# Kernel tuning notes

Hardware: AMD Instinct MI355X
Metric: run time of the kernel (lower is better)

Reference implementation:

```python
import jax, jax.numpy as jnp
import numpy as np

D, H, DK, L, FF = 512, 8, 64, 6, 2048
MAXREL = 512
R = 2 * MAXREL + 1
B, S = 4, 512


def _ln(x, g, b):
    m = jnp.mean(x, -1, keepdims=True)
    v = jnp.mean((x - m) ** 2, -1, keepdims=True)
    return (x - m) * jax.lax.rsqrt(v + 1e-5) * g + b


def _gelu(x):
    return jax.nn.gelu(x, approximate=False)


def setup_inputs() -> dict:
    key = jax.random.key(0)
    ks = iter(jax.random.split(key, 64))
    def rnd(shape, scale=0.02):
        return jax.random.normal(next(ks), shape, jnp.float32) * scale
    inp = {"x": jax.random.normal(next(ks), (B, S, D), jnp.float32)}
    # SeasonalDecomposition params (3 seasonal nets stacked on leading axis)
    inp.update(
        sd_t1_w=rnd((D, D)), sd_t1_b=jnp.zeros((D,), jnp.float32),
        sd_t2_w=rnd((D, D)), sd_t2_b=jnp.zeros((D,), jnp.float32),
        sd_s1_w=rnd((3, D, D // 2)), sd_s1_b=jnp.zeros((3, D // 2), jnp.float32),
        sd_s2_w=rnd((3, D // 2, D)), sd_s2_b=jnp.zeros((3, D), jnp.float32),
        sd_r1_w=rnd((D, D // 2)), sd_r1_b=jnp.zeros((D // 2,), jnp.float32),
        sd_r2_w=rnd((D // 2, D)), sd_r2_b=jnp.zeros((D,), jnp.float32),
        sd_comb=jnp.ones((5,), jnp.float32),
        # 6 TemporalFusionTransformer layers, params stacked on leading axis L
        wq=rnd((L, D, D)), wk=rnd((L, D, D)), wv=rnd((L, D, D)),
        wo_w=rnd((L, D, D)), wo_b=jnp.zeros((L, D), jnp.float32),
        rel_k=rnd((L, R, DK), 1.0), rel_v=rnd((L, R, DK), 1.0),
        ln_attn_g=jnp.ones((L, D), jnp.float32), ln_attn_b=jnp.zeros((L, D), jnp.float32),
        ff1_w=rnd((L, D, FF)), ff1_b=jnp.zeros((L, FF), jnp.float32),
        ff2_w=rnd((L, FF, D)), ff2_b=jnp.zeros((L, D), jnp.float32),
        n1_g=jnp.ones((L, D), jnp.float32), n1_b=jnp.zeros((L, D), jnp.float32),
        n2_g=jnp.ones((L, D), jnp.float32), n2_b=jnp.zeros((L, D), jnp.float32),
    )
    return inp


def _forward(x, sd_t1_w, sd_t1_b, sd_t2_w, sd_t2_b, sd_s1_w, sd_s1_b, sd_s2_w, sd_s2_b,
             sd_r1_w, sd_r1_b, sd_r2_w, sd_r2_b, sd_comb,
             wq, wk, wv, wo_w, wo_b, rel_k, rel_v, ln_attn_g, ln_attn_b,
             ff1_w, ff1_b, ff2_w, ff2_b, n1_g, n1_b, n2_g, n2_b):
    b, s, d = x.shape
    # relative position index matrix, rp[i, j] = clip(j - i) + MAXREL
    r = jnp.arange(s)
    rp = jnp.clip(r[None, :] - r[:, None], -MAXREL, MAXREL) + MAXREL  # [S, S]

    # ---- SeasonalDecomposition (eval mode: dropout = identity) ----
    trend = _gelu(x @ sd_t1_w + sd_t1_b) @ sd_t2_w + sd_t2_b
    h = _gelu(jnp.einsum('bsd,kdm->kbsm', x, sd_s1_w) + sd_s1_b[:, None, None, :])
    seas = jnp.einsum('kbsm,kmd->kbsd', h, sd_s2_w) + sd_s2_b[:, None, None, :]  # [3,B,S,D]
    resid = _gelu(x @ sd_r1_w + sd_r1_b) @ sd_r2_w + sd_r2_b
    w = jax.nn.softmax(sd_comb)
    x = w[0] * trend + w[4] * resid + jnp.einsum('k,kbsd->bsd', w[1:4], seas)

    scale = np.float32(1.0 / np.sqrt(DK))

    def layer(xc, p):
        q = (xc @ p['wq']).reshape(b, s, H, DK).transpose(0, 2, 1, 3)  # [B,H,S,DK]
        k = (xc @ p['wk']).reshape(b, s, H, DK).transpose(0, 2, 1, 3)
        v = (xc @ p['wv']).reshape(b, s, H, DK).transpose(0, 2, 1, 3)
        scores = jnp.einsum('bhid,bhjd->bhij', q, k) * scale
        rk = p['rel_k'][rp]  # [S,S,DK] gathered rel-pos key bias
        scores = scores + jnp.einsum('bhid,ijd->bhij', q, rk)
        a = jax.nn.softmax(scores, axis=-1)
        ctx = jnp.einsum('bhij,bhjd->bhid', a, v)
        rv = p['rel_v'][rp]  # [S,S,DK]
        ctx = ctx + jnp.einsum('bhij,ijd->bhid', a, rv)
        ctx = ctx.transpose(0, 2, 1, 3).reshape(b, s, d)
        out = ctx @ p['wo_w'] + p['wo_b']
        attn = _ln(out + xc, p['ln_attn_g'], p['ln_attn_b'])
        y = _ln(xc + attn, p['n1_g'], p['n1_b'])
        ff = _gelu(y @ p['ff1_w'] + p['ff1_b']) @ p['ff2_w'] + p['ff2_b']
        y = _ln(y + ff, p['n2_g'], p['n2_b'])
        return y, None

    layers = dict(wq=wq, wk=wk, wv=wv, wo_w=wo_w, wo_b=wo_b, rel_k=rel_k, rel_v=rel_v,
                  ln_attn_g=ln_attn_g, ln_attn_b=ln_attn_b,
                  ff1_w=ff1_w, ff1_b=ff1_b, ff2_w=ff2_w, ff2_b=ff2_b,
                  n1_g=n1_g, n1_b=n1_b, n2_g=n2_g, n2_b=n2_b)
    x, _ = jax.lax.scan(layer, x, layers)
    return x


def reference(x, sd_t1_w, sd_t1_b, sd_t2_w, sd_t2_b, sd_s1_w, sd_s1_b, sd_s2_w, sd_s2_b,
              sd_r1_w, sd_r1_b, sd_r2_w, sd_r2_b, sd_comb,
              wq, wk, wv, wo_w, wo_b, rel_k, rel_v, ln_attn_g, ln_attn_b,
              ff1_w, ff1_b, ff2_w, ff2_b, n1_g, n1_b, n2_g, n2_b):
    return _forward(x, sd_t1_w, sd_t1_b, sd_t2_w, sd_t2_b, sd_s1_w, sd_s1_b, sd_s2_w, sd_s2_b,
                    sd_r1_w, sd_r1_b, sd_r2_w, sd_r2_b, sd_comb,
                    wq, wk, wv, wo_w, wo_b, rel_k, rel_v, ln_attn_g, ln_attn_b,
                    ff1_w, ff1_b, ff2_w, ff2_b, n1_g, n1_b, n2_g, n2_b)
```

## Files before the change

### kernel.cpp

```cpp
#include <hip/hip_runtime.h>
#include <hip/hip_bf16.h>

typedef __attribute__((ext_vector_type(4))) float f32x4;
typedef __attribute__((ext_vector_type(8))) short bf16x8;
typedef __attribute__((ext_vector_type(4))) short bf16x4;

#define NL 6

static __device__ __forceinline__ unsigned short f2bf(float f) {
    __hip_bfloat16 h = __float2bfloat16(f);
    return *reinterpret_cast<unsigned short*>(&h);
}
static __device__ __forceinline__ float bf2f(unsigned short u) {
    union { unsigned int u32; float f; } c; c.u32 = ((unsigned int)u) << 16; return c.f;
}
static __device__ __forceinline__ float gelu_exact(float v) {
    return 0.5f * v * (1.0f + erff(v * 0.70710678118654752f));
}
static __device__ __forceinline__ void gload_lds16(const void* g, void* l) {
    __builtin_amdgcn_global_load_lds((const __attribute__((address_space(1))) void*)g,
                                     (__attribute__((address_space(3))) void*)l, 16, 0, 0);
}
static __device__ __forceinline__ f32x4 MF(bf16x8 a, bf16x8 b, f32x4 c) {
    return __builtin_amdgcn_mfma_f32_16x16x32_bf16(a, b, c, 0, 0, 0);
}

template<int BM, int BN, bool OBF, bool BIAS, bool GACT, bool SPART, bool DUAL>
__global__ __launch_bounds__(256)
void gemm3(const unsigned short* __restrict__ A, const unsigned short* __restrict__ B,
           void* __restrict__ C, unsigned short* __restrict__ C2,
           const float* __restrict__ bias,
           int M, int N, int nkt, int skN, int lda, int ldb, int ldc, float alpha,
           int modA, long sA1, long sA2, int modB, long sB1, long sB2,
           int modC, long sC1, long sC2, int biasStride, long pStride)
{
    constexpr int MI = BM / 32, NI = BN / 32;
    constexpr int ACH = BM / 8, NCH = (BM + BN) / 8;
    __shared__ __attribute__((aligned(16))) unsigned short Ls[(BM + BN) * 64];

    const int bz = blockIdx.z;
    const int sk = SPART ? (bz % skN) : 0;
    const int z  = SPART ? (bz / skN) : bz;
    const unsigned short* Ab = A + (long)(z % modA) * sA1 + (long)(z / modA) * sA2;
    const unsigned short* Bb = B + (long)(z % modB) * sB1 + (long)(z / modB) * sB2;
    const long offC = (long)(z % modC) * sC1 + (long)(z / modC) * sC2;

    const int bm0 = blockIdx.x * BM, bn0 = blockIdx.y * BN;
    const int t = threadIdx.x, lane = t & 63, w = t >> 6;
    const int wm = (w >> 1) * (BM / 2), wn = (w & 1) * (BN / 2);
    const int crow8 = lane >> 3, cs8 = lane & 7;
    const int fr = lane & 15, kq = lane >> 4;
    const int kBase = sk * nkt * 64;

    f32x4 acc[MI][NI];
    #pragma unroll
    for (int a = 0; a < MI; a++)
        #pragma unroll
        for (int b = 0; b < NI; b++) acc[a][b] = (f32x4){0.f, 0.f, 0.f, 0.f};

    for (int kt = 0; kt < nkt; ++kt) {
        const int k0 = kBase + (kt << 6);
        #pragma unroll
        for (int c0 = 0; c0 < NCH; c0 += 4) {
            int c = c0 + w;
            if (c < NCH) {
                const unsigned short* gp;
                if (c < ACH) {
                    int rit = c * 8 + crow8;
                    int ks = cs8 ^ (rit & 7);
                    gp = Ab + (long)(bm0 + rit) * lda + k0 + ks * 8;
                } else {
                    int rit = (c - ACH) * 8 + crow8;
                    int ks = cs8 ^ (rit & 7);
                    gp = Bb + (long)(bn0 + rit) * ldb + k0 + ks * 8;
                }
                gload_lds16(gp, &Ls[c * 512]);
            }
        }
        __syncthreads();
        bf16x8 af[2][MI], bfr[2][NI];
        #pragma unroll
        for (int mi = 0; mi < MI; mi++) {
            int R = wm + mi * 16 + fr;
            af[0][mi] = *(const bf16x8*)&Ls[R * 64 + ((kq ^ (R & 7)) << 3)];
            af[1][mi] = *(const bf16x8*)&Ls[R * 64 + (((4 + kq) ^ (R & 7)) << 3)];
        }
        #pragma unroll
        for (int ni = 0; ni < NI; ni++) {
            int Rb = wn + ni * 16 + fr;
            bfr[0][ni] = *(const bf16x8*)&Ls[BM * 64 + Rb * 64 + ((kq ^ (Rb & 7)) << 3)];
            bfr[1][ni] = *(const bf16x8*)&Ls[BM * 64 + Rb * 64 + (((4 + kq) ^ (Rb & 7)) << 3)];
        }
        #pragma unroll
        for (int kh = 0; kh < 2; kh++)
            #pragma unroll
            for (int mi = 0; mi < MI; mi++)
                #pragma unroll
                for (int ni = 0; ni < NI; ni++)
                    acc[mi][ni] = MF(af[kh][mi], bfr[kh][ni], acc[mi][ni]);
        __syncthreads();
    }

    const int q4 = (lane >> 4) << 2;
    if (SPART) {
        float* P = (float*)C + sk * pStride + offC;
        #pragma unroll
        for (int mi = 0; mi < MI; mi++)
            #pragma unroll
            for (int ni = 0; ni < NI; ni++)
                #pragma unroll
                for (int j = 0; j < 4; j++) {
                    int gr = bm0 + wm + mi * 16 + q4 + j;
                    int gc = bn0 + wn + ni * 16 + fr;
                    if (gc < N) P[(long)gr * ldc + gc] = acc[mi][ni][j] * alpha;
                }
    } else {
        float* Cf = (float*)C + offC;
        unsigned short* Ch = (unsigned short*)C + offC;
        unsigned short* C2h = DUAL ? (C2 + offC) : nullptr;
        const float* bp = BIAS ? (bias + (long)z * biasStride) : nullptr;
        #pragma unroll
        for (int mi = 0; mi < MI; mi++)
            #pragma unroll
            for (int ni = 0; ni < NI; ni++)
                #pragma unroll
                for (int j = 0; j < 4; j++) {
                    int gr = bm0 + wm + mi * 16 + q4 + j;
                    int gc = bn0 + wn + ni * 16 + fr;
                    if (gc < N) {
                        float v = acc[mi][ni][j] * alpha;
                        if (BIAS) v += bp[gc];
                        if (GACT) v = gelu_exact(v);
                        if (OBF) Ch[(long)gr * ldc + gc] = f2bf(v);
                        else     Cf[(long)gr * ldc + gc] = v;
                        if (DUAL) C2h[(long)gr * ldc + gc] = f2bf(v);
                    }
                }
    }
}

__global__ __launch_bounds__(256)
void fused_attn2(const unsigned short* __restrict__ qkv,
                 const unsigned short* __restrict__ vt,
                 const unsigned short* __restrict__ rk,
                 const unsigned short* __restrict__ rvt,
                 unsigned short* __restrict__ ctx)
{
    __shared__ __attribute__((aligned(16))) unsigned short L[65536];
    const int bh = blockIdx.y, b = bh >> 3, h = bh & 7;
    const int i0 = blockIdx.x * 64;
    const int t = threadIdx.x, lane = t & 63, wv = t >> 6;
    const int crow = lane >> 2, cs = lane & 3;
    const int fr = lane & 15, kq = lane >> 4;
    const int q4 = kq << 2;
    const int iiw = wv * 16;
    const int PB = 53248, GA = 57344;

    const unsigned short* Qg = qkv + ((long)(b * 512 + i0)) * 1536 + h * 64;
    const unsigned short* Kg = qkv + ((long)(b * 512)) * 1536 + 512 + h * 64;
    const unsigned short* Vg = vt + ((long)bh * 64) * 512;

    auto stage = [&](int jt, int sbuf) {
        const int j0 = jt * 64, rbase = j0 - i0 + 448;
        const int SB = 4096 + sbuf * 24576;
        #pragma unroll
        for (int k = 0; k < 12; k++) {
            int c = wv + k * 4;
            const unsigned short* gp; int dst;
            if (c < 8) {
                int kt = c >> 2, row = (c & 3) * 16 + crow, ks = cs ^ (row & 3);
                gp = Kg + (long)(j0 + row) * 1536 + kt * 32 + ks * 8;
                dst = SB + c * 512;
            } else if (c < 16) {
                int cc = c - 8;
                int kt = cc >> 2, row = (cc & 3) * 16 + crow, ks = cs ^ (row & 3);
                gp = Vg + (long)row * 512 + j0 + kt * 32 + ks * 8;
                dst = SB + 4096 + cc * 512;
            } else if (c < 32) {
                int cc = c - 16;
                int kt = cc >> 2, row = (cc & 3) * 16 + crow, ks = cs ^ (row & 3);
                gp = rvt + (long)row * 1056 + rbase + kt * 32 + ks * 8;
                dst = SB + 8192 + cc * 512;
            } else {
                int cc = c - 32;
                int kt = cc >> 3, row = (cc & 7) * 16 + crow, ks = cs ^ (row & 3);
                gp = rk + (long)(rbase + row) * 64 + kt * 32 + ks * 8;
                dst = SB + 16384 + cc * 512;
            }
            gload_lds16(gp, &L[dst]);
        }
    };

    #pragma unroll
    for (int k = 0; k < 2; k++) {
        int c = wv + k * 4;
        int kt = c >> 2, row = (c & 3) * 16 + crow, ks = cs ^ (row & 3);
        gload_lds16(Qg + (long)row * 1536 + kt * 32 + ks * 8, &L[c * 512]);
    }
    stage(0, 0);
    __syncthreads();
    bf16x8 qf[2];
    {
        int r = iiw + fr;
        qf[0] = *(const bf16x8*)&L[r * 32 + ((kq ^ (r & 3)) << 3)];
        qf[1] = *(const bf16x8*)&L[2048 + r * 32 + ((kq ^ (r & 3)) << 3)];
    }

    f32x4 ctxa[4];
    #pragma unroll
    for (int ni = 0; ni < 4; ni++) ctxa[ni] = (f32x4){0.f, 0.f, 0.f, 0.f};
    float m_[4] = {-1e30f, -1e30f, -1e30f, -1e30f};
    float l_[4] = {0.f, 0.f, 0.f, 0.f};

    for (int jt = 0; jt < 8; ++jt) {
        const int sb = jt & 1;
        const int SB = 4096 + sb * 24576;
        if (jt < 7) stage(jt + 1, sb ^ 1);
        f32x4 gacc[8];
        #pragma unroll
        for (int wb = 0; wb < 8; wb++) {
            int Rb = wb * 16 + fr;
            bf16x8 rk0 = *(const bf16x8*)&L[SB + 16384 + Rb * 32 + ((kq ^ (Rb & 3)) << 3)];
            bf16x8 rk1 = *(const bf16x8*)&L[SB + 20480 + Rb * 32 + ((kq ^ (Rb & 3)) << 3)];
            f32x4 g = (f32x4){0.f, 0.f, 0.f, 0.f};
            g = MF(qf[0], rk0, g);
            gacc[wb] = MF(qf[1], rk1, g);
        }
        #pragma unroll
        for (int wb = 0; wb < 8; wb++)
            #pragma unroll
            for (int j = 0; j < 4; j++) {
                int il = iiw + q4 + j, ww = wb * 16 + fr;
                L[GA + il * 128 + (((ww >> 3) ^ (il & 7)) << 3) + (ww & 7)] = f2bf(gacc[wb][j]);
            }
        f32x4 s[4];
        #pragma unroll
        for (int ni = 0; ni < 4; ni++) {
            int rB = ni * 16 + fr;
            bf16x8 b0 = *(const bf16x8*)&L[SB + rB * 32 + ((kq ^ (rB & 3)) << 3)];
            bf16x8 b1 = *(const bf16x8*)&L[SB + 2048 + rB * 32 + ((kq ^ (rB & 3)) << 3)];
            f32x4 a0 = (f32x4){0.f, 0.f, 0.f, 0.f};
            a0 = MF(qf[0], b0, a0);
            s[ni] = MF(qf[1], b1, a0);
        }
        #pragma unroll
        for (int ni = 0; ni < 4; ni++)
            #pragma unroll
            for (int j = 0; j < 4; j++) {
                int il = iiw + q4 + j;
                int ww = ni * 16 + fr - il + 64;
                s[ni][j] = s[ni][j] * 0.125f
                         + bf2f(L[GA + il * 128 + (((ww >> 3) ^ (il & 7)) << 3) + (ww & 7)]);
            }
        float mx[4];
        #pragma unroll
        for (int j = 0; j < 4; j++) {
            mx[j] = fmaxf(fmaxf(s[0][j], s[1][j]), fmaxf(s[2][j], s[3][j]));
            #pragma unroll
            for (int msk = 1; msk < 16; msk <<= 1) mx[j] = fmaxf(mx[j], __shfl_xor(mx[j], msk));
        }
        float scl[4];
        #pragma unroll
        for (int j = 0; j < 4; j++) {
            float mn = fmaxf(m_[j], mx[j]);
            scl[j] = __expf(m_[j] - mn);
            m_[j] = mn;
        }
        float rs[4] = {0.f, 0.f, 0.f, 0.f};
        #pragma unroll
        for (int ni = 0; ni < 4; ni++)
            #pragma unroll
            for (int j = 0; j < 4; j++) {
                float p = __expf(s[ni][j] - m_[j]);
                s[ni][j] = p;
                rs[j] += p;
            }
        #pragma unroll
        for (int j = 0; j < 4; j++) {
            #pragma unroll
            for (int msk = 1; msk < 16; msk <<= 1) rs[j] += __shfl_xor(rs[j], msk);
            l_[j] = l_[j] * scl[j] + rs[j];
        }
        #pragma unroll
        for (int ni = 0; ni < 4; ni++)
            #pragma unroll
            for (int j = 0; j < 4; j++) ctxa[ni][j] *= scl[j];
        #pragma unroll
        for (int ni = 0; ni < 4; ni++)
            #pragma unroll
            for (int j = 0; j < 4; j++) {
                int il = iiw + q4 + j;
                int jj = ni * 16 + fr;
                unsigned short pb = f2bf(s[ni][j]);
                L[PB + il * 64 + (((jj >> 3) ^ (il & 7)) << 3) + (jj & 7)] = pb;
                int wI = jj - il + 64;
                L[GA + il * 128 + (((wI >> 3) ^ (il & 7)) << 3) + (wI & 7)] = pb;
                int wz = (wI + 64) & 127;
                L[GA + il * 128 + (((wz >> 3) ^ (il & 7)) << 3) + (wz & 7)] = 0;
            }
        const int r = iiw + fr;
        bf16x8 pa0 = *(const bf16x8*)&L[PB + r * 64 + ((kq ^ (r & 7)) << 3)];
        bf16x8 pa1 = *(const bf16x8*)&L[PB + r * 64 + (((4 + kq) ^ (r & 7)) << 3)];
        #pragma unroll
        for (int ni = 0; ni < 4; ni++) {
            int rB = ni * 16 + fr;
            bf16x8 vb0 = *(const bf16x8*)&L[SB + 4096 + rB * 32 + ((kq ^ (rB & 3)) << 3)];
            bf16x8 vb1 = *(const bf16x8*)&L[SB + 6144 + rB * 32 + ((kq ^ (rB & 3)) << 3)];
            ctxa[ni] = MF(pa0, vb0, ctxa[ni]);
            ctxa[ni] = MF(pa1, vb1, ctxa[ni]);
        }
        #pragma unroll
        for (int kt2 = 0; kt2 < 4; kt2++) {
            bf16x8 aa = *(const bf16x8*)&L[GA + r * 128 + (((kt2 * 4 + kq) ^ (r & 7)) << 3)];
            #pragma unroll
            for (int ni = 0; ni < 4; ni++) {
                int rB = ni * 16 + fr;
                bf16x8 rb = *(const bf16x8*)&L[SB + 8192 + kt2 * 2048 + rB * 32 + ((kq ^ (rB & 3)) << 3)];
                ctxa[ni] = MF(aa, rb, ctxa[ni]);
            }
        }
        __syncthreads();
    }
    #pragma unroll
    for (int j = 0; j < 4; j++) {
        float inv = 1.f / l_[j];
        int il = iiw + q4 + j;
        unsigned short* op = ctx + ((long)(b * 512 + i0 + il)) * 512 + h * 64;
        #pragma unroll
        for (int ni = 0; ni < 4; ni++)
            op[ni * 16 + fr] = f2bf(ctxa[ni][j] * inv);
    }
}

__global__ __launch_bounds__(256)
void trcast_k(const float* __restrict__ in, unsigned short* __restrict__ out,
              int R, int C, int ldo, long inStride, long outStride,
              const float* __restrict__ scp, int sczs)
{
    __shared__ unsigned short tile[32][33];
    const int z = blockIdx.z;
    const float* ip = in + (long)z * inStride;
    unsigned short* op = out + (long)z * outStride;
    const float sc = scp ? scp[z * sczs] : 1.0f;
    const int c0 = blockIdx.x * 32, r0 = blockIdx.y * 32;
    const int tx = threadIdx.x & 31, ty = threadIdx.x >> 5;
    #pragma unroll
    for (int q = 0; q < 4; q++) {
        int r = r0 + ty + q * 8;
        float v = (r < R) ? ip[(long)r * C + c0 + tx] * sc : 0.f;
        tile[ty + q * 8][tx] = f2bf(v);
    }
    __syncthreads();
    #pragma unroll
    for (int q = 0; q < 4; q++) {
        int c = c0 + ty + q * 8;
        op[(long)c * ldo + r0 + tx] = tile[tx][ty + q * 8];
    }
}

__global__ __launch_bounds__(256)
void qkvwo_tr(const float* __restrict__ wq, const float* __restrict__ wk,
              const float* __restrict__ wv, const float* __restrict__ wo,
              unsigned short* __restrict__ qkvT, unsigned short* __restrict__ woT)
{
    __shared__ unsigned short tile[32][33];
    const int z = blockIdx.z;
    const int which = z >> 1 >> 1 >> 0;
    const int wsel = z / 6, l = z % 6;
    const float* ip = (wsel == 0 ? wq : wsel == 1 ? wk : wsel == 2 ? wv : wo) + (long)l * 262144;
    unsigned short* op = (wsel < 3) ? (qkvT + (long)l * 786432 + (long)wsel * 262144)
                                    : (woT + (long)l * 262144);
    const int c0 = blockIdx.x * 32, r0 = blockIdx.y * 32;
    const int tx = threadIdx.x & 31, ty = threadIdx.x >> 5;
    #pragma unroll
    for (int q = 0; q < 4; q++)
        tile[ty + q * 8][tx] = f2bf(ip[(long)(r0 + ty + q * 8) * 512 + c0 + tx]);
    __syncthreads();
    #pragma unroll
    for (int q = 0; q < 4; q++)
        op[(long)(c0 + ty + q * 8) * 512 + r0 + tx] = tile[tx][ty + q * 8];
    (void)which;
}

__global__ __launch_bounds__(256)
void castpad_k(const float* __restrict__ in, unsigned short* __restrict__ out,
               int R, int C, long inStride, long outStride, long nPerZ)
{
    const int z = blockIdx.z;
    for (long idx = (long)blockIdx.x * 256 + threadIdx.x; idx < nPerZ;
         idx += (long)gridDim.x * 256) {
        int r = (int)(idx / C);
        float v = (r < R) ? in[(long)z * inStride + idx] : 0.f;
        out[(long)z * outStride + idx] = f2bf(v);
    }
}

__global__ __launch_bounds__(256)
void transp_v(const unsigned short* __restrict__ v, unsigned short* __restrict__ vt, int ldv)
{
    __shared__ unsigned short tile[32][33];
    const int b = blockIdx.z;
    const int j0 = blockIdx.x * 32, c0 = blockIdx.y * 32;
    const int tx = threadIdx.x & 31, ty = threadIdx.x >> 5;
    #pragma unroll
    for (int q = 0; q < 4; q++)
        tile[ty + q * 8][tx] = v[(long)(b * 512 + j0 + ty + q * 8) * ldv + c0 + tx];
    __syncthreads();
    #pragma unroll
    for (int q = 0; q < 4; q++) {
        int c = c0 + ty + q * 8;
        int h = c >> 6, d = c & 63;
        vt[((long)(b * 8 + h) * 64 + d) * 512 + j0 + tx] = tile[tx][ty + q * 8];
    }
}

__global__ __launch_bounds__(256)
void ln2x_k(const float* __restrict__ p0, const float* __restrict__ p1,
            const float* __restrict__ wb, const float* __restrict__ x,
            const float* __restrict__ g1, const float* __restrict__ b1,
            const float* __restrict__ g2, const float* __restrict__ b2,
            float* __restrict__ yf, unsigned short* __restrict__ yb)
{
    const int wv = threadIdx.x >> 6, lane = threadIdx.x & 63;
    const long row = (long)blockIdx.x * 4 + wv;
    const int base = lane * 8;
    const float* pa = p0 + row * 512 + base;
    const float* pbp = p1 + row * 512 + base;
    const float* px = x + row * 512 + base;
    float xv[8], v[8];
    {
        float4 x0 = *(const float4*)px, x1 = *(const float4*)(px + 4);
        float4 a0 = *(const float4*)pa, a1 = *(const float4*)(pa + 4);
        float4 c0 = *(const float4*)pbp, c1 = *(const float4*)(pbp + 4);
        float4 w0 = *(const float4*)(wb + base), w1 = *(const float4*)(wb + base + 4);
        xv[0] = x0.x; xv[1] = x0.y; xv[2] = x0.z; xv[3] = x0.w;
        xv[4] = x1.x; xv[5] = x1.y; xv[6] = x1.z; xv[7] = x1.w;
        v[0] = xv[0] + a0.x + c0.x + w0.x; v[1] = xv[1] + a0.y + c0.y + w0.y;
        v[2] = xv[2] + a0.z + c0.z + w0.z; v[3] = xv[3] + a0.w + c0.w + w0.w;
        v[4] = xv[4] + a1.x + c1.x + w1.x; v[5] = xv[5] + a1.y + c1.y + w1.y;
        v[6] = xv[6] + a1.z + c1.z + w1.z; v[7] = xv[7] + a1.w + c1.w + w1.w;
    }
    float s = 0.f;
    #pragma unroll
    for (int jj = 0; jj < 8; jj++) s += v[jj];
    #pragma unroll
    for (int off = 32; off; off >>= 1) s += __shfl_xor(s, off);
    float mean = s * (1.f / 512.f);
    float vs = 0.f;
    #pragma unroll
    for (int jj = 0; jj < 8; jj++) { float d = v[jj] - mean; vs += d * d; }
    #pragma unroll
    for (int off = 32; off; off >>= 1) vs += __shfl_xor(vs, off);
    float inv = rsqrtf(vs * (1.f / 512.f) + 1e-5f);
    float4 ga = *(const float4*)(g1 + base), gb = *(const float4*)(g1 + base + 4);
    float4 ba = *(const float4*)(b1 + base), bb = *(const float4*)(b1 + base + 4);
    float gg[8] = {ga.x, ga.y, ga.z, ga.w, gb.x, gb.y, gb.z, gb.w};
    float ee[8] = {ba.x, ba.y, ba.z, ba.w, bb.x, bb.y, bb.z, bb.w};
    float tvec[8];
    #pragma unroll
    for (int jj = 0; jj < 8; jj++) tvec[jj] = xv[jj] + (v[jj] - mean) * inv * gg[jj] + ee[jj];
    float s2 = 0.f;
    #pragma unroll
    for (int jj = 0; jj < 8; jj++) s2 += tvec[jj];
    #pragma unroll
    for (int off = 32; off; off >>= 1) s2 += __shfl_xor(s2, off);
    float m2 = s2 * (1.f / 512.f);
    float vs2 = 0.f;
    #pragma unroll
    for (int jj = 0; jj < 8; jj++) { float d = tvec[jj] - m2; vs2 += d * d; }
    #pragma unroll
    for (int off = 32; off; off >>= 1) vs2 += __shfl_xor(vs2, off);
    float inv2 = rsqrtf(vs2 * (1.f / 512.f) + 1e-5f);
    float4 gc = *(const float4*)(g2 + base), gd = *(const float4*)(g2 + base + 4);
    float4 bc = *(const float4*)(b2 + base), bd = *(const float4*)(b2 + base + 4);
    float g2v[8] = {gc.x, gc.y, gc.z, gc.w, gd.x, gd.y, gd.z, gd.w};
    float b2v[8] = {bc.x, bc.y, bc.z, bc.w, bd.x, bd.y, bd.z, bd.w};
    float r[8];
    #pragma unroll
    for (int jj = 0; jj < 8; jj++) r[jj] = (tvec[jj] - m2) * inv2 * g2v[jj] + b2v[jj];
    float* pf = yf + row * 512 + base;
    *(float4*)pf = (float4){r[0], r[1], r[2], r[3]};
    *(float4*)(pf + 4) = (float4){r[4], r[5], r[6], r[7]};
    bf16x8 ov;
    #pragma unroll
    for (int jj = 0; jj < 8; jj++) ov[jj] = (short)f2bf(r[jj]);
    *(bf16x8*)(yb + row * 512 + base) = ov;
}

__global__ __launch_bounds__(256)
void lnff_k(const float* __restrict__ y1, const float* __restrict__ parts,
            const float* __restrict__ bias,
            const float* __restrict__ g, const float* __restrict__ be,
            float* __restrict__ o, unsigned short* __restrict__ ob)
{
    const int wv = threadIdx.x >> 6, lane = threadIdx.x & 63;
    const long row = (long)blockIdx.x * 4 + wv;
    const int base = lane * 8;
    const float* pa = y1 + row * 512 + base;
    float v[8];
    {
        float4 x0 = *(const float4*)pa, x1 = *(const float4*)(pa + 4);
        float4 w0 = *(const float4*)(bias + base), w1 = *(const float4*)(bias + base + 4);
        v[0] = x0.x + w0.x; v[1] = x0.y + w0.y; v[2] = x0.z + w0.z; v[3] = x0.w + w0.w;
        v[4] = x1.x + w1.x; v[5] = x1.y + w1.y; v[6] = x1.z + w1.z; v[7] = x1.w + w1.w;
    }
    #pragma unroll
    for (int k = 0; k < 4; k++) {
        const float* pp = parts + (long)k * 1048576 + row * 512 + base;
        float4 a0 = *(const float4*)pp, a1 = *(const float4*)(pp + 4);
        v[0] += a0.x; v[1] += a0.y; v[2] += a0.z; v[3] += a0.w;
        v[4] += a1.x; v[5] += a1.y; v[6] += a1.z; v[7] += a1.w;
    }
    float s = 0.f;
    #pragma unroll
    for (int jj = 0; jj < 8; jj++) s += v[jj];
    #pragma unroll
    for (int off = 32; off; off >>= 1) s += __shfl_xor(s, off);
    float mean = s * (1.f / 512.f);
    float vs = 0.f;
    #pragma unroll
    for (int jj = 0; jj < 8; jj++) { float d = v[jj] - mean; vs += d * d; }
    #pragma unroll
    for (int off = 32; off; off >>= 1) vs += __shfl_xor(vs, off);
    float inv = rsqrtf(vs * (1.f / 512.f) + 1e-5f);
    float4 g0 = *(const float4*)(g + base), g1 = *(const float4*)(g + base + 4);
    float4 e0 = *(const float4*)(be + base), e1 = *(const float4*)(be + base + 4);
    float gg[8] = {g0.x, g0.y, g0.z, g0.w, g1.x, g1.y, g1.z, g1.w};
    float ee[8] = {e0.x, e0.y, e0.z, e0.w, e1.x, e1.y, e1.z, e1.w};
    float r[8];
    #pragma unroll
    for (int jj = 0; jj < 8; jj++) r[jj] = (v[jj] - mean) * inv * gg[jj] + ee[jj];
    float* po = o + row * 512 + base;
    *(float4*)po = (float4){r[0], r[1], r[2], r[3]};
    *(float4*)(po + 4) = (float4){r[4], r[5], r[6], r[7]};
    bf16x8 ov;
    #pragma unroll
    for (int jj = 0; jj < 8; jj++) ov[jj] = (short)f2bf(r[jj]);
    *(bf16x8*)(ob + row * 512 + base) = ov;
}

__global__ void softmax5_k(const float* __restrict__ comb, float* __restrict__ c5)
{
    if (threadIdx.x == 0 && blockIdx.x == 0) {
        float c[5]; float m = -1e30f;
        for (int k = 0; k < 5; k++) { c[k] = comb[k]; m = fmaxf(m, c[k]); }
        float s = 0.f;
        for (int k = 0; k < 5; k++) { c[k] = __expf(c[k] - m); s += c[k]; }
        for (int k = 0; k < 5; k++) c5[k] = c[k] / s;
    }
}

__global__ __launch_bounds__(256)
void bias_build_k(const float* __restrict__ t1b, const float* __restrict__ r1b,
                  const float* __restrict__ s1b, const float* __restrict__ t2b,
                  const float* __restrict__ r2b, const float* __restrict__ s2b,
                  const float* __restrict__ c5, float* __restrict__ b1c,
                  float* __restrict__ bc)
{
    int i = threadIdx.x + blockIdx.x * 256;
    if (i < 512) b1c[i] = t1b[i];
    else if (i < 768) b1c[i] = r1b[i - 512];
    else if (i < 1536) b1c[i] = s1b[i - 768];
    else if (i < 2048) {
        int n = i - 1536;
        bc[n] = c5[0] * t2b[n] + c5[4] * r2b[n]
              + c5[1] * s2b[n] + c5[2] * s2b[512 + n] + c5[3] * s2b[1024 + n];
    }
}

#define G3(BM,BN,OBF,BIAS,GACT,SPART,DUAL, A,B,C,C2,bias_, M,N,NKT,SKN, lda,ldb,ldc, alpha, mA,a1,a2, mB,b1,b2, mC,c1,c2, bstr, pstr, Zg) \
    gemm3<BM,BN,OBF,BIAS,GACT,SPART,DUAL><<<dim3((M)/(BM), ((N)+(BN)-1)/(BN), (Zg)), dim3(256), 0, stream>>>( \
        (A),(B),(C),(C2),(bias_),(M),(N),(NKT),(SKN),(lda),(ldb),(ldc),(alpha), \
        (mA),(long)(a1),(long)(a2),(mB),(long)(b1),(long)(b2),(mC),(long)(c1),(long)(c2),(bstr),(long)(pstr))

extern "C" void kernel_launch(void* const* d_in, const int* in_sizes, int n_in,
                              void* d_out, int out_size, void* d_ws, size_t ws_size,
                              hipStream_t stream)
{
    (void)in_sizes; (void)n_in; (void)out_size; (void)ws_size;
    const float* x    = (const float*)d_in[0];
    const float* t1w  = (const float*)d_in[1];
    const float* t1b  = (const float*)d_in[2];
    const float* t2w  = (const float*)d_in[3];
    const float* t2b  = (const float*)d_in[4];
    const float* s1w  = (const float*)d_in[5];
    const float* s1b  = (const float*)d_in[6];
    const float* s2w  = (const float*)d_in[7];
    const float* s2b  = (const float*)d_in[8];
    const float* r1w  = (const float*)d_in[9];
    const float* r1b  = (const float*)d_in[10];
    const float* r2w  = (const float*)d_in[11];
    const float* r2b  = (const float*)d_in[12];
    const float* comb = (const float*)d_in[13];
    const float* wq   = (const float*)d_in[14];
    const float* wk   = (const float*)d_in[15];
    const float* wvv  = (const float*)d_in[16];
    const float* wow  = (const float*)d_in[17];
    const float* wob  = (const float*)d_in[18];
    const float* relk = (const float*)d_in[19];
    const float* relv = (const float*)d_in[20];
    const float* lag  = (const float*)d_in[21];
    const float* labi = (const float*)d_in[22];
    const float* f1w  = (const float*)d_in[23];
    const float* f1b  = (const float*)d_in[24];
    const float* f2w  = (const float*)d_in[25];
    const float* f2b  = (const float*)d_in[26];
    const float* n1g  = (const float*)d_in[27];
    const float* n1b  = (const float*)d_in[28];
    const float* n2g  = (const float*)d_in[29];
    const float* n2b  = (const float*)d_in[30];

    char* ws = (char*)d_ws;
    #define OFFK(kb) (ws + (size_t)(kb) * 1024)
    float* X    = (float*)OFFK(0);
    float* T3   = (float*)OFFK(8192);
    float* PART = (float*)OFFK(12288);
    unsigned short* Xb   = (unsigned short*)OFFK(45056);
    unsigned short* Xb0  = (unsigned short*)OFFK(47104);
    unsigned short* QKVb = (unsigned short*)OFFK(49152);
    unsigned short* VT   = (unsigned short*)OFFK(55296);
    unsigned short* CTXb = (unsigned short*)OFFK(57344);
    unsigned short* T3b  = (unsigned short*)OFFK(59392);
    unsigned short* FFb  = (unsigned short*)OFFK(61440);
    unsigned short* W1   = (unsigned short*)OFFK(69632);
    unsigned short* W2   = (unsigned short*)OFFK(71168);
    float* b1c = (float*)OFFK(72704);
    float* bc  = (float*)OFFK(72712);
    float* c5  = (float*)OFFK(72716);
    unsigned short* qkvT = (unsigned short*)OFFK(119808);
    unsigned short* woT  = (unsigned short*)OFFK(129024);
    unsigned short* f1wT = (unsigned short*)OFFK(132096);
    unsigned short* f2wT = (unsigned short*)OFFK(144384);
    unsigned short* relkb= (unsigned short*)OFFK(156672);
    unsigned short* rvT  = (unsigned short*)OFFK(157488);
    unsigned short* Hb   = QKVb;

    castpad_k<<<dim3(1024, 1, 1), 256, 0, stream>>>(x, Xb0, 2048, 512, 1048576, 1048576, 1048576);
    softmax5_k<<<dim3(1), 64, 0, stream>>>(comb, c5);
    bias_build_k<<<dim3(8), 256, 0, stream>>>(t1b, r1b, s1b, t2b, r2b, s2b, c5, b1c, bc);
    trcast_k<<<dim3(16, 16, 1), 256, 0, stream>>>(t1w, W1, 512, 512, 512, 0, 0, nullptr, 0);
    trcast_k<<<dim3(8, 16, 1), 256, 0, stream>>>(r1w, W1 + 262144, 512, 256, 512, 0, 0, nullptr, 0);
    trcast_k<<<dim3(8, 16, 3), 256, 0, stream>>>(s1w, W1 + 393216, 512, 256, 512, 131072, 131072, nullptr, 0);
    trcast_k<<<dim3(16, 16, 1), 256, 0, stream>>>(t2w, W2, 512, 512, 1536, 0, 0, c5, 0);
    trcast_k<<<dim3(16, 8, 1), 256, 0, stream>>>(r2w, W2 + 512, 256, 512, 1536, 0, 0, c5 + 4, 0);
    trcast_k<<<dim3(16, 8, 3), 256, 0, stream>>>(s2w, W2 + 768, 256, 512, 1536, 131072, 256, c5 + 1, 1);
    qkvwo_tr<<<dim3(16, 16, 24), 256, 0, stream>>>(wq, wk, wvv, wow, qkvT, woT);
    trcast_k<<<dim3(64, 16, 6), 256, 0, stream>>>(f1w, f1wT, 512, 2048, 512, 1048576, 1048576, nullptr, 0);
    trcast_k<<<dim3(16, 64, 6), 256, 0, stream>>>(f2w, f2wT, 2048, 512, 2048, 1048576, 1048576, nullptr, 0);
    trcast_k<<<dim3(2, 33, 6), 256, 0, stream>>>(relv, rvT, 1025, 64, 1056, 65600, 67584, nullptr, 0);
    castpad_k<<<dim3(272, 1, 6), 256, 0, stream>>>(relk, relkb, 1025, 64, 65600, 69632, 69632);

    G3(64,64,true,true,true,false,false,  Xb0, W1, Hb, nullptr, b1c, 2048,1536,8,1, 512,512,1536, 1.f,
       1,0,0, 1,0,0, 1,0,0, 0,0, 1);
    G3(64,64,false,true,false,false,true, Hb, W2, X, Xb, bc, 2048,512,24,1, 1536,1536,512, 1.f,
       1,0,0, 1,0,0, 1,0,0, 0,0, 1);

    for (int l = 0; l < NL; ++l) {
        const unsigned short* qkvTl = qkvT + (long)l * 786432;
        const unsigned short* woTl  = woT + (long)l * 262144;
        const unsigned short* f1Tl  = f1wT + (long)l * 1048576;
        const unsigned short* f2Tl  = f2wT + (long)l * 1048576;
        const unsigned short* rkl   = relkb + (long)l * 69632;
        const unsigned short* rvl   = rvT + (long)l * 67584;

        G3(64,64,true,false,false,false,false, Xb, qkvTl, QKVb, nullptr, nullptr, 2048,1536,8,1, 512,512,1536, 1.f,
           1,0,0, 1,0,0, 1,0,0, 0,0, 1);
        transp_v<<<dim3(16, 16, 4), 256, 0, stream>>>(QKVb + 1024, VT, 1536);
        fused_attn2<<<dim3(8, 32), 256, 0, stream>>>(QKVb, VT, rkl, rvl, CTXb);
        G3(64,64,false,false,false,true,false, CTXb, woTl, PART, nullptr, nullptr, 2048,512,4,2, 512,512,512, 1.f,
           1,0,0, 1,0,0, 1,0,0, 0,1048576, 2);
        ln2x_k<<<dim3(512), 256, 0, stream>>>(PART, PART + 1048576, wob + l * 512, X,
                                              lag + l * 512, labi + l * 512,
                                              n1g + l * 512, n1b + l * 512, T3, T3b);
        G3(64,64,true,true,true,false,false, T3b, f1Tl, FFb, nullptr, f1b + l * 2048, 2048,2048,8,1, 512,512,2048, 1.f,
           1,0,0, 1,0,0, 1,0,0, 0,0, 1);
        G3(64,64,false,false,false,true,false, FFb, f2Tl, PART, nullptr, nullptr, 2048,512,8,4, 2048,2048,512, 1.f,
           1,0,0, 1,0,0, 1,0,0, 0,1048576, 4);
        float* outp = (l == NL - 1) ? (float*)d_out : X;
        lnff_k<<<dim3(512), 256, 0, stream>>>(T3, PART, f2b + l * 512,
                                              n2g + l * 512, n2b + l * 512, outp, Xb);
    }
}
```

Measured before the change: 554.1 us.

## Fuse V transpose into QKV GEMM epilogue and read rel tables from global

```diff
diff --git a/kernel.cpp b/kernel.cpp
--- a/kernel.cpp
+++ b/kernel.cpp
@@ -25,7 +25,7 @@
     return __builtin_amdgcn_mfma_f32_16x16x32_bf16(a, b, c, 0, 0, 0);
 }
 
-template<int BM, int BN, bool OBF, bool BIAS, bool GACT, bool SPART, bool DUAL>
+template<int BM, int BN, bool OBF, bool BIAS, bool GACT, bool SPART, bool DUAL, bool VTR>
 __global__ __launch_bounds__(256)
 void gemm3(const unsigned short* __restrict__ A, const unsigned short* __restrict__ B,
            void* __restrict__ C, unsigned short* __restrict__ C2,
@@ -102,7 +102,25 @@
     }
 
     const int q4 = (lane >> 4) << 2;
-    if (SPART) {
+    if (VTR && bn0 >= 1024) {
+        #pragma unroll
+        for (int mi = 0; mi < MI; mi++)
+            #pragma unroll
+            for (int ni = 0; ni < NI; ni++)
+                #pragma unroll
+                for (int j = 0; j < 4; j++) {
+                    int lr = wm + mi * 16 + q4 + j;
+                    int lc = wn + ni * 16 + fr;
+                    Ls[lc * 64 + ((((lr >> 4) ^ (lc & 3)) << 4) | (lr & 15))] = f2bf(acc[mi][ni][j]);
+                }
+        __syncthreads();
+        int dl = t >> 2, c4 = (t & 3) << 4;
+        const unsigned short* src = &Ls[dl * 64 + (((t & 3) ^ (dl & 3)) << 4)];
+        unsigned short* dst = C2 + ((long)((bm0 >> 9) * 8 + ((bn0 - 1024) >> 6)) * 64 + dl) * 512
+                              + (bm0 & 511) + c4;
+        *(bf16x8*)dst = *(const bf16x8*)src;
+        *((bf16x8*)dst + 1) = *((const bf16x8*)src + 1);
+    } else if (SPART) {
         float* P = (float*)C + sk * pStride + offC;
         #pragma unroll
         for (int mi = 0; mi < MI; mi++)
@@ -140,13 +158,13 @@
 }
 
 __global__ __launch_bounds__(256)
-void fused_attn2(const unsigned short* __restrict__ qkv,
+void fused_attn3(const unsigned short* __restrict__ qkv,
                  const unsigned short* __restrict__ vt,
                  const unsigned short* __restrict__ rk,
                  const unsigned short* __restrict__ rvt,
                  unsigned short* __restrict__ ctx)
 {
-    __shared__ __attribute__((aligned(16))) unsigned short L[65536];
+    __shared__ __attribute__((aligned(16))) unsigned short L[32768];
     const int bh = blockIdx.y, b = bh >> 3, h = bh & 7;
     const int i0 = blockIdx.x * 64;
     const int t = threadIdx.x, lane = t & 63, wv = t >> 6;
@@ -154,38 +172,28 @@
     const int fr = lane & 15, kq = lane >> 4;
     const int q4 = kq << 2;
     const int iiw = wv * 16;
-    const int PB = 53248, GA = 57344;
+    const int PB = 20480, GA = 24576;
 
     const unsigned short* Qg = qkv + ((long)(b * 512 + i0)) * 1536 + h * 64;
     const unsigned short* Kg = qkv + ((long)(b * 512)) * 1536 + 512 + h * 64;
     const unsigned short* Vg = vt + ((long)bh * 64) * 512;
 
     auto stage = [&](int jt, int sbuf) {
-        const int j0 = jt * 64, rbase = j0 - i0 + 448;
-        const int SB = 4096 + sbuf * 24576;
-        #pragma unroll
-        for (int k = 0; k < 12; k++) {
+        const int j0 = jt * 64;
+        const int SB = 4096 + sbuf * 8192;
+        #pragma unroll
+        for (int k = 0; k < 4; k++) {
             int c = wv + k * 4;
             const unsigned short* gp; int dst;
             if (c < 8) {
                 int kt = c >> 2, row = (c & 3) * 16 + crow, ks = cs ^ (row & 3);
                 gp = Kg + (long)(j0 + row) * 1536 + kt * 32 + ks * 8;
                 dst = SB + c * 512;
-            } else if (c < 16) {
+            } else {
                 int cc = c - 8;
                 int kt = cc >> 2, row = (cc & 3) * 16 + crow, ks = cs ^ (row & 3);
                 gp = Vg + (long)row * 512 + j0 + kt * 32 + ks * 8;
                 dst = SB + 4096 + cc * 512;
-            } else if (c < 32) {
-                int cc = c - 16;
-                int kt = cc >> 2, row = (cc & 3) * 16 + crow, ks = cs ^ (row & 3);
-                gp = rvt + (long)row * 1056 + rbase + kt * 32 + ks * 8;
-                dst = SB + 8192 + cc * 512;
-            } else {
-                int cc = c - 32;
-                int kt = cc >> 3, row = (cc & 7) * 16 + crow, ks = cs ^ (row & 3);
-                gp = rk + (long)(rbase + row) * 64 + kt * 32 + ks * 8;
-                dst = SB + 16384 + cc * 512;
             }
             gload_lds16(gp, &L[dst]);
         }
@@ -214,14 +222,16 @@
 
     for (int jt = 0; jt < 8; ++jt) {
         const int sb = jt & 1;
-        const int SB = 4096 + sb * 24576;
+        const int SB = 4096 + sb * 8192;
+        const int rbase = jt * 64 - i0 + 448;
         if (jt < 7) stage(jt + 1, sb ^ 1);
         f32x4 gacc[8];
         #pragma unroll
         for (int wb = 0; wb < 8; wb++) {
             int Rb = wb * 16 + fr;
-            bf16x8 rk0 = *(const bf16x8*)&L[SB + 16384 + Rb * 32 + ((kq ^ (Rb & 3)) << 3)];
-            bf16x8 rk1 = *(const bf16x8*)&L[SB + 20480 + Rb * 32 + ((kq ^ (Rb & 3)) << 3)];
+            const unsigned short* rkp = rk + (long)(rbase + Rb) * 64 + kq * 8;
+            bf16x8 rk0 = *(const bf16x8*)rkp;
+            bf16x8 rk1 = *(const bf16x8*)(rkp + 32);
             f32x4 g = (f32x4){0.f, 0.f, 0.f, 0.f};
             g = MF(qf[0], rk0, g);
             gacc[wb] = MF(qf[1], rk1, g);
@@ -298,6 +308,13 @@
                 int wz = (wI + 64) & 127;
                 L[GA + il * 128 + (((wz >> 3) ^ (il & 7)) << 3) + (wz & 7)] = 0;
             }
+        bf16x8 rvf[4][4];
+        #pragma unroll
+        for (int kt2 = 0; kt2 < 4; kt2++)
+            #pragma unroll
+            for (int ni = 0; ni < 4; ni++)
+                rvf[kt2][ni] = *(const bf16x8*)(rvt + (long)(ni * 16 + fr) * 1056
+                                                + rbase + kt2 * 32 + kq * 8);
         const int r = iiw + fr;
         bf16x8 pa0 = *(const bf16x8*)&L[PB + r * 64 + ((kq ^ (r & 7)) << 3)];
         bf16x8 pa1 = *(const bf16x8*)&L[PB + r * 64 + (((4 + kq) ^ (r & 7)) << 3)];
@@ -313,11 +330,8 @@
         for (int kt2 = 0; kt2 < 4; kt2++) {
             bf16x8 aa = *(const bf16x8*)&L[GA + r * 128 + (((kt2 * 4 + kq) ^ (r & 7)) << 3)];
             #pragma unroll
-            for (int ni = 0; ni < 4; ni++) {
-                int rB = ni * 16 + fr;
-                bf16x8 rb = *(const bf16x8*)&L[SB + 8192 + kt2 * 2048 + rB * 32 + ((kq ^ (rB & 3)) << 3)];
-                ctxa[ni] = MF(aa, rb, ctxa[ni]);
-            }
+            for (int ni = 0; ni < 4; ni++)
+                ctxa[ni] = MF(aa, rvf[kt2][ni], ctxa[ni]);
         }
         __syncthreads();
     }
@@ -365,7 +379,6 @@
 {
     __shared__ unsigned short tile[32][33];
     const int z = blockIdx.z;
-    const int which = z >> 1 >> 1 >> 0;
     const int wsel = z / 6, l = z % 6;
     const float* ip = (wsel == 0 ? wq : wsel == 1 ? wk : wsel == 2 ? wv : wo) + (long)l * 262144;
     unsigned short* op = (wsel < 3) ? (qkvT + (long)l * 786432 + (long)wsel * 262144)
@@ -379,7 +392,6 @@
     #pragma unroll
     for (int q = 0; q < 4; q++)
         op[(long)(c0 + ty + q * 8) * 512 + r0 + tx] = tile[tx][ty + q * 8];
-    (void)which;
 }
 
 __global__ __launch_bounds__(256)
@@ -392,25 +404,6 @@
         int r = (int)(idx / C);
         float v = (r < R) ? in[(long)z * inStride + idx] : 0.f;
         out[(long)z * outStride + idx] = f2bf(v);
-    }
-}
-
-__global__ __launch_bounds__(256)
-void transp_v(const unsigned short* __restrict__ v, unsigned short* __restrict__ vt, int ldv)
-{
-    __shared__ unsigned short tile[32][33];
-    const int b = blockIdx.z;
-    const int j0 = blockIdx.x * 32, c0 = blockIdx.y * 32;
-    const int tx = threadIdx.x & 31, ty = threadIdx.x >> 5;
-    #pragma unroll
-    for (int q = 0; q < 4; q++)
-        tile[ty + q * 8][tx] = v[(long)(b * 512 + j0 + ty + q * 8) * ldv + c0 + tx];
-    __syncthreads();
-    #pragma unroll
-    for (int q = 0; q < 4; q++) {
-        int c = c0 + ty + q * 8;
-        int h = c >> 6, d = c & 63;
-        vt[((long)(b * 8 + h) * 64 + d) * 512 + j0 + tx] = tile[tx][ty + q * 8];
     }
 }
 
@@ -568,8 +561,8 @@
     }
 }
 
-#define G3(BM,BN,OBF,BIAS,GACT,SPART,DUAL, A,B,C,C2,bias_, M,N,NKT,SKN, lda,ldb,ldc, alpha, mA,a1,a2, mB,b1,b2, mC,c1,c2, bstr, pstr, Zg) \
-    gemm3<BM,BN,OBF,BIAS,GACT,SPART,DUAL><<<dim3((M)/(BM), ((N)+(BN)-1)/(BN), (Zg)), dim3(256), 0, stream>>>( \
+#define G3(BM,BN,OBF,BIAS,GACT,SPART,DUAL,VTR, A,B,C,C2,bias_, M,N,NKT,SKN, lda,ldb,ldc, alpha, mA,a1,a2, mB,b1,b2, mC,c1,c2, bstr, pstr, Zg) \
+    gemm3<BM,BN,OBF,BIAS,GACT,SPART,DUAL,VTR><<<dim3((M)/(BM), ((N)+(BN)-1)/(BN), (Zg)), dim3(256), 0, stream>>>( \
         (A),(B),(C),(C2),(bias_),(M),(N),(NKT),(SKN),(lda),(ldb),(ldc),(alpha), \
         (mA),(long)(a1),(long)(a2),(mB),(long)(b1),(long)(b2),(mC),(long)(c1),(long)(c2),(bstr),(long)(pstr))
 
@@ -650,9 +643,9 @@
     trcast_k<<<dim3(2, 33, 6), 256, 0, stream>>>(relv, rvT, 1025, 64, 1056, 65600, 67584, nullptr, 0);
     castpad_k<<<dim3(272, 1, 6), 256, 0, stream>>>(relk, relkb, 1025, 64, 65600, 69632, 69632);
 
-    G3(64,64,true,true,true,false,false,  Xb0, W1, Hb, nullptr, b1c, 2048,1536,8,1, 512,512,1536, 1.f,
+    G3(64,64,true,true,true,false,false,false,  Xb0, W1, Hb, nullptr, b1c, 2048,1536,8,1, 512,512,1536, 1.f,
        1,0,0, 1,0,0, 1,0,0, 0,0, 1);
-    G3(64,64,false,true,false,false,true, Hb, W2, X, Xb, bc, 2048,512,24,1, 1536,1536,512, 1.f,
+    G3(64,64,false,true,false,false,true,false, Hb, W2, X, Xb, bc, 2048,512,24,1, 1536,1536,512, 1.f,
        1,0,0, 1,0,0, 1,0,0, 0,0, 1);
 
     for (int l = 0; l < NL; ++l) {
@@ -663,18 +656,17 @@
         const unsigned short* rkl   = relkb + (long)l * 69632;
         const unsigned short* rvl   = rvT + (long)l * 67584;
 
-        G3(64,64,true,false,false,false,false, Xb, qkvTl, QKVb, nullptr, nullptr, 2048,1536,8,1, 512,512,1536, 1.f,
+        G3(64,64,true,false,false,false,false,true, Xb, qkvTl, QKVb, VT, nullptr, 2048,1536,8,1, 512,512,1536, 1.f,
            1,0,0, 1,0,0, 1,0,0, 0,0, 1);
-        transp_v<<<dim3(16, 16, 4), 256, 0, stream>>>(QKVb + 1024, VT, 1536);
-        fused_attn2<<<dim3(8, 32), 256, 0, stream>>>(QKVb, VT, rkl, rvl, CTXb);
-        G3(64,64,false,false,false,true,false, CTXb, woTl, PART, nullptr, nullptr, 2048,512,4,2, 512,512,512, 1.f,
+        fused_attn3<<<dim3(8, 32), 256, 0, stream>>>(QKVb, VT, rkl, rvl, CTXb);
+        G3(64,64,false,false,false,true,false,false, CTXb, woTl, PART, nullptr, nullptr, 2048,512,4,2, 512,512,512, 1.f,
            1,0,0, 1,0,0, 1,0,0, 0,1048576, 2);
         ln2x_k<<<dim3(512), 256, 0, stream>>>(PART, PART + 1048576, wob + l * 512, X,
                                               lag + l * 512, labi + l * 512,
                                               n1g + l * 512, n1b + l * 512, T3, T3b);
-        G3(64,64,true,true,true,false,false, T3b, f1Tl, FFb, nullptr, f1b + l * 2048, 2048,2048,8,1, 512,512,2048, 1.f,
+        G3(64,64,true,true,true,false,false,false, T3b, f1Tl, FFb, nullptr, f1b + l * 2048, 2048,2048,8,1, 512,512,2048, 1.f,
            1,0,0, 1,0,0, 1,0,0, 0,0, 1);
-        G3(64,64,false,false,false,true,false, FFb, f2Tl, PART, nullptr, nullptr, 2048,512,8,4, 2048,2048,512, 1.f,
+        G3(64,64,false,false,false,true,false,false, FFb, f2Tl, PART, nullptr, nullptr, 2048,512,8,4, 2048,2048,512, 1.f,
            1,0,0, 1,0,0, 1,0,0, 0,1048576, 4);
         float* outp = (l == NL - 1) ? (float*)d_out : X;
         lnff_k<<<dim3(512), 256, 0, stream>>>(T3, PART, f2b + l * 512,
```

Result: slower. 596.1 us (+7.6%).
